# Kernel optimization log

Measured on AMD Instinct MI355X. Metric: run time of the kernel, lower is better.

Reference implementation:

```python
import jax, jax.numpy as jnp
import numpy as np

QLEN, MLEN, BSZ = 1024, 1024, 2
D_MODEL, N_HEAD, D_HEAD, D_INNER = 1024, 16, 64, 4096
KLEN = QLEN + MLEN
RLEN = KLEN + QLEN
EPS = 1e-12
SCALE = 1.0 / np.sqrt(D_HEAD).astype(np.float32)
STD = 0.02


def gelu(x):
    # OpenAI-GPT tanh-approx gelu used by XLNet
    return 0.5 * x * (1.0 + jnp.tanh(np.sqrt(2.0 / np.pi) * (x + 0.044715 * x ** 3)))


def layer_norm(x, g, b):
    m = jnp.mean(x, axis=-1, keepdims=True)
    v = jnp.mean((x - m) ** 2, axis=-1, keepdims=True)
    return (x - m) * jax.lax.rsqrt(v + EPS) * g + b


def rel_shift(x, klen):
    # x: [qlen, rlen, bsz, n_head] -> [qlen, klen, bsz, n_head]
    q, r, b, n = x.shape
    x = jnp.reshape(x, (r, q, b, n))[1:]
    x = jnp.reshape(x, (q, r - 1, b, n))[:, :klen]
    return x


def setup_inputs() -> dict:
    key = jax.random.key(0)
    ks = jax.random.split(key, 16)
    h = jax.random.normal(ks[0], (QLEN, BSZ, D_MODEL), jnp.float32)
    mems = jax.random.normal(ks[1], (MLEN, BSZ, D_MODEL), jnp.float32)
    r = jax.random.normal(ks[2], (RLEN, BSZ, D_MODEL), jnp.float32)
    # segment one-hot: 1 if query and key segments differ (XLNet convention)
    qseg = jax.random.randint(ks[3], (QLEN, BSZ), 0, 2)
    kseg = jax.random.randint(ks[4], (KLEN, BSZ), 0, 2)
    seg_mat = jax.nn.one_hot((qseg[:, None, :] != kseg[None, :, :]).astype(jnp.int32), 2, dtype=jnp.float32)  # [q,k,b,2]
    # causal mask with mems: query i may attend to key j <= i + MLEN
    i = jnp.arange(QLEN)[:, None]
    j = jnp.arange(KLEN)[None, :]
    attn_mask = (j > i + MLEN).astype(jnp.float32)[:, :, None, None]  # [q,k,1,1]
    wq = jax.random.normal(ks[5], (D_MODEL, N_HEAD, D_HEAD), jnp.float32) * STD
    wk = jax.random.normal(ks[6], (D_MODEL, N_HEAD, D_HEAD), jnp.float32) * STD
    wv = jax.random.normal(ks[7], (D_MODEL, N_HEAD, D_HEAD), jnp.float32) * STD
    wo = jax.random.normal(ks[8], (D_MODEL, N_HEAD, D_HEAD), jnp.float32) * STD
    wr = jax.random.normal(ks[9], (D_MODEL, N_HEAD, D_HEAD), jnp.float32) * STD
    r_w_bias = jnp.zeros((N_HEAD, D_HEAD), jnp.float32)
    r_r_bias = jnp.zeros((N_HEAD, D_HEAD), jnp.float32)
    r_s_bias = jnp.zeros((N_HEAD, D_HEAD), jnp.float32)
    seg_embed = jax.random.normal(ks[10], (2, N_HEAD, D_HEAD), jnp.float32) * STD
    ln_attn_g = jnp.ones((D_MODEL,), jnp.float32)
    ln_attn_b = jnp.zeros((D_MODEL,), jnp.float32)
    w1 = jax.random.normal(ks[11], (D_MODEL, D_INNER), jnp.float32) * STD
    b1 = jnp.zeros((D_INNER,), jnp.float32)
    w2 = jax.random.normal(ks[12], (D_INNER, D_MODEL), jnp.float32) * STD
    b2 = jnp.zeros((D_MODEL,), jnp.float32)
    ln_ff_g = jnp.ones((D_MODEL,), jnp.float32)
    ln_ff_b = jnp.zeros((D_MODEL,), jnp.float32)
    return dict(h=h, mems=mems, r=r, seg_mat=seg_mat, attn_mask=attn_mask,
                wq=wq, wk=wk, wv=wv, wo=wo, wr=wr,
                r_w_bias=r_w_bias, r_r_bias=r_r_bias, r_s_bias=r_s_bias, seg_embed=seg_embed,
                ln_attn_g=ln_attn_g, ln_attn_b=ln_attn_b,
                w1=w1, b1=b1, w2=w2, b2=b2, ln_ff_g=ln_ff_g, ln_ff_b=ln_ff_b)


def reference(h, mems, r, seg_mat, attn_mask, wq, wk, wv, wo, wr,
              r_w_bias, r_r_bias, r_s_bias, seg_embed,
              ln_attn_g, ln_attn_b, w1, b1, w2, b2, ln_ff_g, ln_ff_b):
    # content-stream XLNet relative attention (g=None path) + FFN
    cat = jnp.concatenate([mems, h], axis=0)            # [klen,b,h]
    q_h = jnp.einsum('ibh,hnd->ibnd', h, wq)
    k_h = jnp.einsum('ibh,hnd->ibnd', cat, wk)
    v_h = jnp.einsum('ibh,hnd->ibnd', cat, wv)
    k_r = jnp.einsum('ibh,hnd->ibnd', r, wr)
    ac = jnp.einsum('ibnd,jbnd->ijbn', q_h + r_w_bias, k_h)
    bd = jnp.einsum('ibnd,jbnd->ijbn', q_h + r_r_bias, k_r)
    bd = rel_shift(bd, KLEN)
    ef = jnp.einsum('ibnd,snd->ibns', q_h + r_s_bias, seg_embed)
    ef = jnp.einsum('ijbs,ibns->ijbn', seg_mat, ef)
    attn_score = (ac + bd + ef) * SCALE - 1e30 * attn_mask
    attn_prob = jax.nn.softmax(attn_score, axis=1)
    attn_vec = jnp.einsum('ijbn,jbnd->ibnd', attn_prob, v_h)
    attn_out = jnp.einsum('ibnd,hnd->ibh', attn_vec, wo) + h
    out_h = layer_norm(attn_out, ln_attn_g, ln_attn_b)
    ff = gelu(out_h @ w1 + b1) @ w2 + b2
    return layer_norm(ff + out_h, ln_ff_g, ln_ff_b)
```

## Files before the change

kernel.cpp:

```cpp
#include <hip/hip_runtime.h>
#include <hip/hip_bf16.h>


#define QLEN 1024
#define MLEN 1024
#define DM 1024
#define NH 16
#define DH 64
#define DI 4096
#define KLEN 2048
#define RLEN 3072

typedef __attribute__((ext_vector_type(8))) short s16x8;
typedef __attribute__((ext_vector_type(4))) float f32x4;
typedef unsigned short us;

__device__ __forceinline__ float bf2f(us u) {
    union { unsigned int i; float f; } x; x.i = ((unsigned int)u) << 16; return x.f;
}
__device__ __forceinline__ us f2bf(float f) {
    union { float f; unsigned int i; } x; x.f = f;
    return (us)((x.i + 0x7fffu + ((x.i >> 16) & 1u)) >> 16);
}
__device__ __forceinline__ void gload16(const void* g, void* lds) {
    __builtin_amdgcn_global_load_lds(
        (const __attribute__((address_space(1))) unsigned int*)g,
        (__attribute__((address_space(3))) unsigned int*)lds, 16, 0, 0);
}

template<bool ISMAX>
__device__ __forceinline__ float block_reduce(float v, float* red, int t) {
    #pragma unroll
    for (int off = 32; off > 0; off >>= 1) {
        float o = __shfl_down(v, off);
        v = ISMAX ? fmaxf(v, o) : (v + o);
    }
    if ((t & 63) == 0) red[t >> 6] = v;
    __syncthreads();
    if (t == 0) {
        float s = red[0];
        #pragma unroll
        for (int w = 1; w < 4; ++w) s = ISMAX ? fmaxf(s, red[w]) : (s + red[w]);
        red[4] = s;
    }
    __syncthreads();
    return red[4];
}

__global__ __launch_bounds__(256) void prep_k(
    const float* __restrict__ mems, const float* __restrict__ h,
    const float* __restrict__ r, const float* __restrict__ wo,
    const float* __restrict__ wq, const float* __restrict__ wk,
    const float* __restrict__ wv, const float* __restrict__ wr,
    const float* __restrict__ w1, const float* __restrict__ w2,
    const float* __restrict__ seg,
    us* __restrict__ cat_bf, us* __restrict__ r_bf, us* __restrict__ wo_b,
    us* __restrict__ wqkv_t, us* __restrict__ wr_t,
    us* __restrict__ w1_t, us* __restrict__ w2_t, us* __restrict__ ksb)
{
    __shared__ us tbuf[64][65];
    int bid = blockIdx.x;
    const int tid = threadIdx.x;
    if (bid < 5632) {
        int t = bid * 256 + tid;
        const float* src; us* dst; int off;
        if (t < 262144)       { src = mems; dst = cat_bf;           off = t; }
        else if (t < 524288)  { src = h;    dst = cat_bf + 2097152; off = t - 262144; }
        else if (t < 1310720) { src = r;    dst = r_bf;             off = t - 524288; }
        else                  { src = wo;   dst = wo_b;             off = t - 1310720; }
        const float4* p = (const float4*)src + 2 * (size_t)off;
        float4 a = p[0], b = p[1];
        us o[8] = { f2bf(a.x), f2bf(a.y), f2bf(a.z), f2bf(a.w),
                    f2bf(b.x), f2bf(b.y), f2bf(b.z), f2bf(b.w) };
        *((uint4*)dst + off) = *(const uint4*)o;
        return;
    }
    bid -= 5632;
    if (bid >= 3072) {
        int t = (bid - 3072) * 256 + tid;
        int bb = t >> 11, j = t & 2047;
        ksb[t] = f2bf(seg[(size_t)j * 4 + bb * 2 + 1]);
        return;
    }
    const float* in; us* out; int R, C, c0, r0;
    if (bid < 1024) {
        int z = bid >> 8, u = bid & 255;
        in  = (z == 0) ? wq : (z == 1) ? wk : (z == 2) ? wv : wr;
        out = (z < 3) ? (wqkv_t + (size_t)z * 1048576) : wr_t;
        R = 1024; C = 1024; c0 = (u & 15) * 64; r0 = (u >> 4) * 64;
    } else if (bid < 2048) {
        int u = bid - 1024;
        in = w1; out = w1_t; R = 1024; C = 4096;
        c0 = (u & 63) * 64; r0 = (u >> 6) * 64;
    } else {
        int u = bid - 2048;
        in = w2; out = w2_t; R = 4096; C = 1024;
        c0 = (u & 15) * 64; r0 = (u >> 4) * 64;
    }
    #pragma unroll
    for (int u = 0; u < 16; ++u) {
        int idx = tid + 256 * u;
        int rr = idx >> 6, cc = idx & 63;
        tbuf[cc][rr] = f2bf(in[(size_t)(r0 + rr) * C + c0 + cc]);
    }
    __syncthreads();
    #pragma unroll
    for (int u = 0; u < 16; ++u) {
        int idx = tid + 256 * u;
        int rr = idx >> 6, cc = idx & 63;
        out[(size_t)(c0 + rr) * R + r0 + cc] = tbuf[rr][cc];
    }
}

__device__ __forceinline__ int offe(int r, int c) {
    return ((r >> 4) * 2 + (c >> 5)) * 512 + (r & 15) * 32 + ((c & 31) ^ ((r & 8) ? 16 : 0));
}

template<int EPI>
__device__ __forceinline__ void gemm8_core(
    const us* __restrict__ A, const us* __restrict__ Bt,
    const float* __restrict__ bias, void* __restrict__ Cout,
    int N, int K, int kbeg, size_t zoff, bool zfirst,
    int bx, int by, us* __restrict__ As8, us* __restrict__ Bs8)
{
    const int tid = threadIdx.x;
    const int w = tid >> 6, l = tid & 63;
    const int lm = l & 15, lg = l >> 4;
    const int wm = w >> 2, wn = w & 3;
    const int m0 = by * 256, n0 = bx * 256;

    int srow[2], scol[2];
    #pragma unroll
    for (int u = 0; u < 2; ++u) {
        int sub = w * 2 + u;
        srow[u] = (sub >> 1) * 16 + (l >> 2);
        scol[u] = (sub & 1) * 32 + (((l & 3) * 8) ^ ((l & 32) ? 16 : 0));
    }

    auto stagePart = [&](int kt1, int P, int db) {
        const us* src = (P < 2) ? (A + (size_t)(m0 + P * 128) * K)
                                : (Bt + (size_t)(n0 + (P - 2) * 128) * K);
        us* dst = ((P < 2) ? As8 : Bs8) + (db * 2 + (P & 1)) * 8192;
        int kc = kbeg + kt1 * 64;
        #pragma unroll
        for (int u = 0; u < 2; ++u)
            gload16(src + (size_t)srow[u] * K + kc + scol[u], dst + (w * 2 + u) * 512);
    };

    f32x4 acc[8][4] = {};
    s16x8 rA0[4][2], rA1[4][2], rB[2][2];

    stagePart(0, 0, 0); stagePart(0, 1, 0); stagePart(0, 2, 0); stagePart(0, 3, 0);

    for (int kt = 0; kt < 16; ++kt) {
        const int d = kt & 1;
        asm volatile("s_waitcnt vmcnt(0)" ::: "memory");
        __builtin_amdgcn_s_barrier();
        asm volatile("" ::: "memory");
        const bool hn = (kt + 1 < 16);
        const us* Ab = As8 + (d * 2 + wm) * 8192;
        const us* Bb = Bs8 + (d * 2 + (wn >> 1)) * 8192;

        if (hn) stagePart(kt + 1, 0, d ^ 1);
        #pragma unroll
        for (int mf2 = 0; mf2 < 4; ++mf2)
            #pragma unroll
            for (int kk = 0; kk < 2; ++kk)
                rA0[mf2][kk] = *(const s16x8*)&Ab[offe(mf2 * 16 + lm, kk * 32 + lg * 8)];
        #pragma unroll
        for (int nf2 = 0; nf2 < 2; ++nf2)
            #pragma unroll
            for (int kk = 0; kk < 2; ++kk)
                rB[nf2][kk] = *(const s16x8*)&Bb[offe((wn & 1) * 64 + nf2 * 16 + lm, kk * 32 + lg * 8)];
        __builtin_amdgcn_s_setprio(1);
        #pragma unroll
        for (int mf2 = 0; mf2 < 4; ++mf2)
            #pragma unroll
            for (int nf2 = 0; nf2 < 2; ++nf2)
                #pragma unroll
                for (int kk = 0; kk < 2; ++kk)
                    acc[mf2][nf2] = __builtin_amdgcn_mfma_f32_16x16x32_bf16(
                        rA0[mf2][kk], rB[nf2][kk], acc[mf2][nf2], 0, 0, 0);
        __builtin_amdgcn_s_setprio(0);

        if (hn) stagePart(kt + 1, 1, d ^ 1);
        #pragma unroll
        for (int mf2 = 0; mf2 < 4; ++mf2)
            #pragma unroll
            for (int kk = 0; kk < 2; ++kk)
                rA1[mf2][kk] = *(const s16x8*)&Ab[offe(64 + mf2 * 16 + lm, kk * 32 + lg * 8)];
        __builtin_amdgcn_s_setprio(1);
        #pragma unroll
        for (int mf2 = 0; mf2 < 4; ++mf2)
            #pragma unroll
            for (int nf2 = 0; nf2 < 2; ++nf2)
                #pragma unroll
                for (int kk = 0; kk < 2; ++kk)
                    acc[4 + mf2][nf2] = __builtin_amdgcn_mfma_f32_16x16x32_bf16(
                        rA1[mf2][kk], rB[nf2][kk], acc[4 + mf2][nf2], 0, 0, 0);
        __builtin_amdgcn_s_setprio(0);

        if (hn) stagePart(kt + 1, 2, d ^ 1);
        #pragma unroll
        for (int nf2 = 0; nf2 < 2; ++nf2)
            #pragma unroll
            for (int kk = 0; kk < 2; ++kk)
                rB[nf2][kk] = *(const s16x8*)&Bb[offe((wn & 1) * 64 + (2 + nf2) * 16 + lm, kk * 32 + lg * 8)];
        __builtin_amdgcn_s_setprio(1);
        #pragma unroll
        for (int mf2 = 0; mf2 < 4; ++mf2)
            #pragma unroll
            for (int nf2 = 0; nf2 < 2; ++nf2)
                #pragma unroll
                for (int kk = 0; kk < 2; ++kk)
                    acc[4 + mf2][2 + nf2] = __builtin_amdgcn_mfma_f32_16x16x32_bf16(
                        rA1[mf2][kk], rB[nf2][kk], acc[4 + mf2][2 + nf2], 0, 0, 0);
        __builtin_amdgcn_s_setprio(0);

        if (hn) stagePart(kt + 1, 3, d ^ 1);
        __builtin_amdgcn_s_setprio(1);
        #pragma unroll
        for (int mf2 = 0; mf2 < 4; ++mf2)
            #pragma unroll
            for (int nf2 = 0; nf2 < 2; ++nf2)
                #pragma unroll
                for (int kk = 0; kk < 2; ++kk)
                    acc[mf2][2 + nf2] = __builtin_amdgcn_mfma_f32_16x16x32_bf16(
                        rA0[mf2][kk], rB[nf2][kk], acc[mf2][2 + nf2], 0, 0, 0);
        __builtin_amdgcn_s_setprio(0);
    }

    #pragma unroll
    for (int mf = 0; mf < 8; ++mf) {
        #pragma unroll
        for (int nf = 0; nf < 4; ++nf) {
            #pragma unroll
            for (int rr = 0; rr < 4; ++rr) {
                int row = m0 + wm * 128 + mf * 16 + lg * 4 + rr;
                int col = n0 + wn * 64 + nf * 16 + lm;
                float v = acc[mf][nf][rr];
                if (EPI == 3) {
                    int s = row >> 1, bb = row & 1, nn = col >> 6, dd = col & 63;
                    ((us*)Cout)[(((size_t)(bb * 16 + nn)) * RLEN + s) * 64 + dd] = f2bf(v);
                } else {
                    int which = col >> 10;
                    int nn = (col >> 6) & 15, dd = col & 63, bb = row & 1;
                    us val = f2bf(v);
                    us* base = (us*)Cout;
                    if (which == 0) {
                        if (row >= 2048)
                            base[(((size_t)(bb * 16 + nn)) * 1024 + ((row - 2048) >> 1)) * 64 + dd] = val;
                    } else if (which == 1) {
                        int j = row >> 1;
                        int jt = j >> 6, ff = (j >> 4) & 3, lmw = j & 15;
                        int ks2 = dd >> 5, lg2 = (dd >> 3) & 3, e2 = dd & 7;
                        (base + 2097152)[((((size_t)(bb * 16 + nn)) * 32 + jt) * 8 + ff * 2 + ks2) * 512
                                         + (lg2 * 16 + lmw) * 8 + e2] = val;
                    } else {
                        int j = row >> 1;
                        int jt = j >> 6, ks2 = (j >> 5) & 1, lg2 = (j >> 3) & 3, e2 = j & 7;
                        int df = dd >> 4, lmw = dd & 15;
                        (base + 6291456)[((((size_t)(bb * 16 + nn)) * 32 + jt) * 8 + df * 2 + ks2) * 512
                                         + (lg2 * 16 + lmw) * 8 + e2] = val;
                    }
                }
            }
        }
    }
}

__global__ __launch_bounds__(512) void proj8_k(
    const us* __restrict__ cat_bf, const us* __restrict__ wqkv_t,
    const us* __restrict__ r_bf, const us* __restrict__ wr_t,
    us* __restrict__ qkv_out, us* __restrict__ kr_out)
{
    __shared__ __align__(16) us As8[2 * 2 * 8192];
    __shared__ __align__(16) us Bs8[2 * 2 * 8192];
    int bid = blockIdx.x;
    if (bid < 192) {
        int swz = (bid & 7) * 24 + (bid >> 3);
        gemm8_core<4>(cat_bf, wqkv_t, nullptr, qkv_out, 3072, 1024, 0,
                      0, true, swz % 12, swz / 12, As8, Bs8);
    } else {
        int idx = bid - 192;
        gemm8_core<3>(r_bf, wr_t, nullptr, kr_out, 1024, 1024, 0,
                      0, true, idx % 4, idx / 4, As8, Bs8);
    }
}

template<int TM, int EPI>
__device__ __forceinline__ void gemm_core(
    const us* __restrict__ A, const us* __restrict__ Bt,
    const float* __restrict__ bias, void* __restrict__ Cout,
    int N, int K, int kbeg, int kchunk, size_t zoff, bool zfirst,
    int bx, int by, us* __restrict__ As, us* __restrict__ Bs)
{
    constexpr int MF = TM / 32;
    constexpr int AISS = TM / 64;
    const int tid = threadIdx.x;
    const int w = tid >> 6, l = tid & 63;
    const int lm = l & 15, lg = l >> 4;
    const int m0 = by * TM, n0 = bx * 128;
    const int wr = (w >> 1) * (TM / 2), wc = (w & 1) * 64;
    const int nt = kchunk / 32;

    f32x4 acc[MF][4] = {};

    auto stage = [&](int buf, int k0) {
        #pragma unroll
        for (int u = 0; u < AISS; ++u) {
            int c = (u * 4 + w) * 64 + l;
            int row = c & (TM - 1), kc = c >> (TM == 128 ? 7 : 6);
            gload16(A + (size_t)(m0 + row) * K + k0 + kc * 8,
                    As + buf * (TM * 32) + (u * 4 + w) * 512);
        }
        #pragma unroll
        for (int u = 0; u < 2; ++u) {
            int c = (u * 4 + w) * 64 + l;
            int row = c & 127, kc = c >> 7;
            gload16(Bt + (size_t)(n0 + row) * K + k0 + kc * 8,
                    Bs + buf * 4096 + (u * 4 + w) * 512);
        }
    };

    stage(0, kbeg);
    int cur = 0;
    for (int t = 0; t < nt; ++t) {
        asm volatile("s_waitcnt vmcnt(0)" ::: "memory");
        __builtin_amdgcn_s_barrier();
        asm volatile("" ::: "memory");
        if (t + 1 < nt) stage(cur ^ 1, kbeg + (t + 1) * 32);

        s16x8 af[MF], bfr[4];
        #pragma unroll
        for (int mf = 0; mf < MF; ++mf)
            af[mf] = *(const s16x8*)&As[cur * (TM * 32) + (lg * TM + wr + mf * 16 + lm) * 8];
        #pragma unroll
        for (int nf = 0; nf < 4; ++nf)
            bfr[nf] = *(const s16x8*)&Bs[cur * 4096 + (lg * 128 + wc + nf * 16 + lm) * 8];
        #pragma unroll
        for (int mf = 0; mf < MF; ++mf)
            #pragma unroll
            for (int nf = 0; nf < 4; ++nf)
                acc[mf][nf] = __builtin_amdgcn_mfma_f32_16x16x32_bf16(
                    af[mf], bfr[nf], acc[mf][nf], 0, 0, 0);
        cur ^= 1;
    }

    #pragma unroll
    for (int mf = 0; mf < MF; ++mf) {
        #pragma unroll
        for (int nf = 0; nf < 4; ++nf) {
            #pragma unroll
            for (int rr = 0; rr < 4; ++rr) {
                int row = m0 + wr + mf * 16 + lg * 4 + rr;
                int col = n0 + wc + nf * 16 + lm;
                float v = acc[mf][nf][rr];
                if (EPI == 1 || (EPI == 2 && zfirst)) v += bias[col];
                if (EPI == 1) {
                    float targ = 0.7978845608028654f * (v + 0.044715f * v * v * v);
                    v = 0.5f * v * (1.0f + tanhf(targ));
                    ((us*)Cout)[(size_t)row * N + col] = f2bf(v);
                } else {
                    ((float*)Cout + zoff)[(size_t)row * N + col] = v;
                }
            }
        }
    }
}

template<int TM, int EPI>
__global__ __launch_bounds__(256) void gemm2(
    const us* __restrict__ A, const us* __restrict__ Bt,
    const float* __restrict__ bias, void* __restrict__ Cout,
    int N, int K, int kchunk, size_t zstride)
{
    __shared__ us As[2 * TM * 32];
    __shared__ us Bs[2 * 128 * 32];
    int lin = blockIdx.y * gridDim.x + blockIdx.x;
    int nwg = gridDim.x * gridDim.y;
    int swz = (lin & 7) * (nwg >> 3) + (lin >> 3);
    int bx = swz % gridDim.x, by = swz / gridDim.x;
    gemm_core<TM, EPI>(A, Bt, bias, Cout, N, K, blockIdx.z * kchunk, kchunk,
                       (size_t)blockIdx.z * zstride, blockIdx.z == 0, bx, by, As, Bs);
}

__global__ __launch_bounds__(256) void attn8_k(
    const us* __restrict__ qb, const us* __restrict__ kfr, const us* __restrict__ vfr,
    const us* __restrict__ krb, const us* __restrict__ ksb,
    const float* __restrict__ rwb, const float* __restrict__ rrb,
    const float* __restrict__ rsb, const float* __restrict__ se,
    const float* __restrict__ seg,
    us* __restrict__ av)
{
    __shared__ us KR_lds[2][128 * 64];
    __shared__ float G_lds[4 * 80 * 20];
    __shared__ us P_lds[4 * 16 * 64];
    __shared__ us KS_lds[2048];
    __shared__ float Qx_lds[64][2];

    const int tid = threadIdx.x;
    const int w = tid >> 6, l = tid & 63;
    const int lm = l & 15, lg = l >> 4;
    int lin = blockIdx.y * gridDim.x + blockIdx.x;
    int swz = (lin & 7) * 64 + (lin >> 3);
    const int i0 = (swz & 15) * 64;
    const int bn = swz >> 4;
    const int b = bn >> 4, n = bn & 15;
    const int i = i0 + w * 16 + lm;

    const float SC = 0.125f * 1.44269504088896340736f;

    const us* kbase = kfr + (size_t)bn * 131072;
    const us* vbase = vfr + (size_t)bn * 131072;

    {
        const us* qrow = qb + ((size_t)bn * QLEN + i0 + l) * DH;
        s16x8 qv8[8];
        #pragma unroll
        for (int c = 0; c < 8; ++c) qv8[c] = *(const s16x8*)(qrow + c * 8);
        float e0 = 0.f, e1 = 0.f;
        #pragma unroll
        for (int c = 0; c < 8; ++c)
            #pragma unroll
            for (int e = 0; e < 8; ++e) {
                int d = c * 8 + e;
                float qv = bf2f((us)qv8[c][e]) + rsb[n * DH + d];
                e0 = fmaf(qv, se[(0 * NH + n) * DH + d], e0);
                e1 = fmaf(qv, se[(1 * NH + n) * DH + d], e1);
            }
        float qsI = seg[(size_t)(i0 + l) * 8192 + b * 2 + 1];
        float qs0 = seg[b * 2 + 1];
        float qs = (qsI != qs0) ? 1.f : 0.f;
        float ed = e1 - e0;
        if (w == 0) {
            Qx_lds[l][0] = (e0 + qs * ed) * SC;
            Qx_lds[l][1] = ed * (1.f - 2.f * qs) * SC;
        }
    }
    __syncthreads();

    s16x8 qwf[2], qrf[2], qxf;
    {
        const us* qrow = qb + ((size_t)bn * QLEN + i) * DH;
        #pragma unroll
        for (int ks = 0; ks < 2; ++ks) {
            s16x8 v = *(const s16x8*)(qrow + ks * 32 + lg * 8);
            #pragma unroll
            for (int e = 0; e < 8; ++e) {
                int d = ks * 32 + lg * 8 + e;
                float f = bf2f((us)v[e]);
                qwf[ks][e] = (short)f2bf((f + rwb[n * DH + d]) * SC);
                qrf[ks][e] = (short)f2bf((f + rrb[n * DH + d]) * SC);
            }
        }
        #pragma unroll
        for (int e = 0; e < 8; ++e) qxf[e] = 0;
        if (lg == 0) {
            qxf[0] = (short)f2bf(Qx_lds[w * 16 + lm][0]);
            qxf[1] = (short)f2bf(Qx_lds[w * 16 + lm][1]);
        }
    }

    auto stageKR = [&](int buf, int j0) {
        const int ur0 = QLEN - i0 - 63 + j0;
        #pragma unroll
        for (int u = 0; u < 4; ++u) {
            int c = (w * 4 + u) * 64 + l;
            int row = c >> 3, ch = c & 7;
            gload16(krb + ((size_t)bn * RLEN + ur0 + row) * DH + ((ch ^ (row & 7)) * 8),
                    &KR_lds[buf][(w * 4 + u) * 512]);
        }
    };

    int njt = ((i0 + 63 + MLEN) >> 6) + 1;
    if (njt > 32) njt = 32;

    gload16(ksb + b * KLEN + (w * 64 + l) * 8, &KS_lds[w * 512]);
    stageKR(0, 0);

    f32x4 of[4] = {{0,0,0,0},{0,0,0,0},{0,0,0,0},{0,0,0,0}};
    float M = -3.0e38f, L = 0.f;
    float* gw = &G_lds[w * 1600];
    us* pw = &P_lds[w * 1024];
    int cur = 0;

    for (int jt = 0; jt < njt; ++jt) {
        const int j0 = jt * 64;
        asm volatile("s_waitcnt vmcnt(0)" ::: "memory");
        __builtin_amdgcn_s_barrier();
        asm volatile("" ::: "memory");
        if (jt + 1 < njt) stageKR(cur ^ 1, j0 + 64);

        s16x8 kf[4][2], vf[4][2];
        #pragma unroll
        for (int f = 0; f < 4; ++f) {
            #pragma unroll
            for (int ks = 0; ks < 2; ++ks) {
                kf[f][ks] = *(const s16x8*)(kbase + (size_t)(((jt * 4 + f) * 2 + ks) * 64 + l) * 8);
                vf[f][ks] = *(const s16x8*)(vbase + (size_t)(((jt * 4 + f) * 2 + ks) * 64 + l) * 8);
            }
        }

        __builtin_amdgcn_s_setprio(1);
        const int woff = 48 - w * 16;
        #pragma unroll
        for (int pf = 0; pf < 5; ++pf) {
            f32x4 g = {0, 0, 0, 0};
            int row = woff + pf * 16 + lm;
            #pragma unroll
            for (int ks = 0; ks < 2; ++ks) {
                s16x8 a = *(const s16x8*)&KR_lds[cur][row * 64 + (((ks * 64 + lg * 16) ^ ((row & 7) << 4)) >> 1)];
                g = __builtin_amdgcn_mfma_f32_16x16x32_bf16(a, qrf[ks], g, 0, 0, 0);
            }
            #pragma unroll
            for (int rr = 0; rr < 4; ++rr)
                gw[(pf * 16 + lg * 4 + rr) * 20 + lm] = g[rr];
        }
        f32x4 sf[4];
        #pragma unroll
        for (int f = 0; f < 4; ++f) {
            f32x4 cfr = {0, 0, 0, 0};
            cfr = __builtin_amdgcn_mfma_f32_16x16x32_bf16(kf[f][0], qwf[0], cfr, 0, 0, 0);
            cfr = __builtin_amdgcn_mfma_f32_16x16x32_bf16(kf[f][1], qwf[1], cfr, 0, 0, 0);
            s16x8 aext;
            #pragma unroll
            for (int e = 0; e < 8; ++e) aext[e] = 0;
            if (lg == 0) {
                aext[0] = (short)0x3F80;
                aext[1] = (short)KS_lds[j0 + f * 16 + lm];
            }
            cfr = __builtin_amdgcn_mfma_f32_16x16x32_bf16(aext, qxf, cfr, 0, 0, 0);
            sf[f] = cfr;
        }
        __builtin_amdgcn_s_setprio(0);

        float sv[16];
        #pragma unroll
        for (int f = 0; f < 4; ++f)
            #pragma unroll
            for (int rr = 0; rr < 4; ++rr) {
                int jl = f * 16 + lg * 4 + rr;
                sv[f * 4 + rr] = sf[f][rr] + gw[(jl + 15 - lm) * 20 + lm];
            }
        if (j0 + 63 > i0 + w * 16 + MLEN) {
            #pragma unroll
            for (int f = 0; f < 4; ++f)
                #pragma unroll
                for (int rr = 0; rr < 4; ++rr) {
                    int jl = f * 16 + lg * 4 + rr;
                    if (j0 + jl > i + MLEN) sv[f * 4 + rr] = -1.0e30f;
                }
        }
        float tmax = sv[0];
        #pragma unroll
        for (int u = 1; u < 16; ++u) tmax = fmaxf(tmax, sv[u]);
        tmax = fmaxf(tmax, __shfl_xor(tmax, 16));
        tmax = fmaxf(tmax, __shfl_xor(tmax, 32));
        float Mnew = fmaxf(M, tmax);
        float scale;
        asm("v_exp_f32 %0, %1" : "=v"(scale) : "v"(M - Mnew));
        float psum = 0.f;
        unsigned int pk[8];
        #pragma unroll
        for (int f = 0; f < 4; ++f) {
            #pragma unroll
            for (int rp = 0; rp < 2; ++rp) {
                float p0, p1;
                asm("v_exp_f32 %0, %1" : "=v"(p0) : "v"(sv[f * 4 + rp * 2] - Mnew));
                asm("v_exp_f32 %0, %1" : "=v"(p1) : "v"(sv[f * 4 + rp * 2 + 1] - Mnew));
                psum += p0 + p1;
                unsigned int pkv;
                asm("v_cvt_pk_bf16_f32 %0, %1, %2" : "=v"(pkv) : "v"(p0), "v"(p1));
                pk[f * 2 + rp] = pkv;
            }
        }
        psum += __shfl_xor(psum, 16);
        psum += __shfl_xor(psum, 32);
        L = L * scale + psum;
        M = Mnew;
        float rs4[4];
        #pragma unroll
        for (int rr = 0; rr < 4; ++rr)
            rs4[rr] = __shfl(scale, (l & 48) | (lg * 4 + rr));
        #pragma unroll
        for (int df = 0; df < 4; ++df)
            #pragma unroll
            for (int rr = 0; rr < 4; ++rr)
                of[df][rr] *= rs4[rr];
        #pragma unroll
        for (int f = 0; f < 4; ++f) {
            #pragma unroll
            for (int rp = 0; rp < 2; ++rp) {
                int jl2 = f * 16 + lg * 4 + rp * 2;
                *(unsigned int*)&pw[lm * 64 + (((jl2 * 2) ^ ((lm & 7) << 4)) >> 1)] = pk[f * 2 + rp];
            }
        }
        __builtin_amdgcn_s_setprio(1);
        #pragma unroll
        for (int ks = 0; ks < 2; ++ks) {
            s16x8 pa = *(const s16x8*)&pw[lm * 64 + (((ks * 64 + lg * 16) ^ ((lm & 7) << 4)) >> 1)];
            #pragma unroll
            for (int df = 0; df < 4; ++df)
                of[df] = __builtin_amdgcn_mfma_f32_16x16x32_bf16(pa, vf[df][ks], of[df], 0, 0, 0);
        }
        __builtin_amdgcn_s_setprio(0);
        cur ^= 1;
    }

    float rl4[4];
    #pragma unroll
    for (int rr = 0; rr < 4; ++rr)
        rl4[rr] = __shfl(L, (l & 48) | (lg * 4 + rr));
    #pragma unroll
    for (int df = 0; df < 4; ++df) {
        #pragma unroll
        for (int rr = 0; rr < 4; ++rr) {
            int m2 = lg * 4 + rr;
            int d = df * 16 + lm;
            int irow = i0 + w * 16 + m2;
            av[((size_t)irow * 2 + b) * DM + n * DH + d] = f2bf(of[df][rr] / rl4[rr]);
        }
    }
}

template<int NSUM, bool RESBF, bool OUTBF>
__global__ __launch_bounds__(256) void ln_k(
    const float* __restrict__ a, const void* __restrict__ resid,
    const float* __restrict__ g, const float* __restrict__ bb,
    void* __restrict__ out)
{
    __shared__ float xs[DM];
    __shared__ float red[5];
    const int r = blockIdx.x;
    const int t = threadIdx.x;
    float lsum = 0.f;
    #pragma unroll
    for (int u = 0; u < 4; ++u) {
        int hdx = t + 256 * u;
        float x = RESBF ? bf2f(((const us*)resid)[(size_t)r * DM + hdx])
                        : ((const float*)resid)[(size_t)r * DM + hdx];
        #pragma unroll
        for (int s = 0; s < NSUM; ++s)
            x += a[(size_t)s * 2097152 + (size_t)r * DM + hdx];
        xs[hdx] = x;
        lsum += x;
    }
    float m = block_reduce<false>(lsum, red, t) * (1.0f / DM);
    float lv = 0.f;
    #pragma unroll
    for (int u = 0; u < 4; ++u) {
        int hdx = t + 256 * u;
        float dd = xs[hdx] - m;
        lv += dd * dd;
    }
    float var = block_reduce<false>(lv, red, t) * (1.0f / DM);
    float rs = rsqrtf(var + 1e-12f);
    #pragma unroll
    for (int u = 0; u < 4; ++u) {
        int hdx = t + 256 * u;
        float y = (xs[hdx] - m) * rs * g[hdx] + bb[hdx];
        if (OUTBF) ((us*)out)[(size_t)r * DM + hdx] = f2bf(y);
        else       ((float*)out)[(size_t)r * DM + hdx] = y;
    }
}

extern "C" void kernel_launch(void* const* d_in, const int* in_sizes, int n_in,
                              void* d_out, int out_size, void* d_ws, size_t ws_size,
                              hipStream_t stream) {
    const float* h         = (const float*)d_in[0];
    const float* mems      = (const float*)d_in[1];
    const float* r         = (const float*)d_in[2];
    const float* seg_mat   = (const float*)d_in[3];
    const float* wq        = (const float*)d_in[5];
    const float* wk        = (const float*)d_in[6];
    const float* wv        = (const float*)d_in[7];
    const float* wo        = (const float*)d_in[8];
    const float* wr        = (const float*)d_in[9];
    const float* rwb       = (const float*)d_in[10];
    const float* rrb       = (const float*)d_in[11];
    const float* rsb       = (const float*)d_in[12];
    const float* seg_embed = (const float*)d_in[13];
    const float* ln_g      = (const float*)d_in[14];
    const float* ln_b      = (const float*)d_in[15];
    const float* w1        = (const float*)d_in[16];
    const float* b1        = (const float*)d_in[17];
    const float* w2        = (const float*)d_in[18];
    const float* b2        = (const float*)d_in[19];
    const float* lf_g      = (const float*)d_in[20];
    const float* lf_b      = (const float*)d_in[21];
    float* out = (float*)d_out;
    char* W = (char*)d_ws;
    const size_t MB = 1ull << 20;

    us*    cat_bf = (us*)(W);
    us*    r_bf   = (us*)(W + 8  * MB);
    us*    wqkv_t = (us*)(W + 20 * MB);
    us*    wr_t   = (us*)(W + 26 * MB);
    us*    wo_b   = (us*)(W + 28 * MB);
    us*    w1_t   = (us*)(W + 30 * MB);
    us*    w2_t   = (us*)(W + 38 * MB);
    us*    q_bf   = (us*)(W + 46 * MB);
    us*    kfrag  = q_bf + 2097152;
    us*    vfrag  = q_bf + 6291456;
    us*    kr_bf  = (us*)(W + 66 * MB);
    us*    av_bf  = (us*)(W + 78 * MB);
    us*    ks_bf  = (us*)(W + 82 * MB);
    us*    oh_bf  = (us*)(W + 83 * MB);
    float* ao     = (float*)(W + 8 * MB);
    us*    ff1_bf = (us*)(W + 46 * MB);
    float* ff2    = (float*)(W);

    dim3 blk(256);
    dim3 blk8(512);
    prep_k<<<dim3(8720), blk, 0, stream>>>(mems, h, r, wo, wq, wk, wv, wr, w1, w2, seg_mat,
                                           cat_bf, r_bf, wo_b, wqkv_t, wr_t, w1_t, w2_t, ks_bf);
    proj8_k<<<dim3(260), blk8, 0, stream>>>(cat_bf, wqkv_t, r_bf, wr_t, q_bf, kr_bf);
    attn8_k<<<dim3(16, 32), blk, 0, stream>>>(q_bf, kfrag, vfrag, kr_bf, ks_bf,
                                              rwb, rrb, rsb, seg_embed, seg_mat, av_bf);
    gemm2<64, 0><<<dim3(8, 32, 2), blk, 0, stream>>>(av_bf, wo_b, nullptr, ao, 1024, 1024, 512, 2097152);
    ln_k<2, false, true><<<dim3(2048), blk, 0, stream>>>(ao, h, ln_g, ln_b, oh_bf);
    gemm2<128, 1><<<dim3(32, 16), blk, 0, stream>>>(oh_bf, w1_t, b1, ff1_bf, 4096, 1024, 1024, 0);
    gemm2<64, 2><<<dim3(8, 32, 4), blk, 0, stream>>>(ff1_bf, w2_t, b2, ff2, 1024, 4096, 1024, 2097152);
    ln_k<4, true, false><<<dim3(2048), blk, 0, stream>>>(ff2, oh_bf, lf_g, lf_b, out);
}
```

Before: 306.3 us.

## Write k_r in MFMA fragment layout and read it directly in attention

The r-projection epilogue now stores k_r pre-shuffled into 16-row MFMA fragment groups, offset by the rel-shift. The attention kernel can then load positional-key fragments straight from global memory, which removes the double-buffered LDS staging of k_r and its per-tile barriers. The attention grid is also flattened and reordered so paired blocks take complementary causal tile counts, for better load balance. The risk is that k_r fragments are now re-read from global/L2 by every block without LDS reuse, and the proj grid changes from 260 to 264 blocks.

```diff
diff --git a/kernel.cpp b/kernel.cpp
--- a/kernel.cpp
+++ b/kernel.cpp
@@ -241,7 +241,12 @@
                 float v = acc[mf][nf][rr];
                 if (EPI == 3) {
                     int s = row >> 1, bb = row & 1, nn = col >> 6, dd = col & 63;
-                    ((us*)Cout)[(((size_t)(bb * 16 + nn)) * RLEN + s) * 64 + dd] = f2bf(v);
+                    if (s >= 1) {
+                        int g = (s - 1) >> 4, lmw = (s - 1) & 15;
+                        int ks2 = dd >> 5, lg2 = (dd >> 3) & 3, e2 = dd & 7;
+                        ((us*)Cout)[((((size_t)(bb * 16 + nn)) * 144 + g) * 2 + ks2) * 512
+                                    + (lg2 * 16 + lmw) * 8 + e2] = f2bf(v);
+                    }
                 } else {
                     int which = col >> 10;
                     int nn = (col >> 6) & 15, dd = col & 63, bb = row & 1;
@@ -272,7 +277,7 @@
 __global__ __launch_bounds__(512) void proj8_k(
     const us* __restrict__ cat_bf, const us* __restrict__ wqkv_t,
     const us* __restrict__ r_bf, const us* __restrict__ wr_t,
-    us* __restrict__ qkv_out, us* __restrict__ kr_out)
+    us* __restrict__ qkv_out, us* __restrict__ krf_out)
 {
     __shared__ __align__(16) us As8[2 * 2 * 8192];
     __shared__ __align__(16) us Bs8[2 * 2 * 8192];
@@ -283,8 +288,8 @@
                       0, true, swz % 12, swz / 12, As8, Bs8);
     } else {
         int idx = bid - 192;
-        gemm8_core<3>(r_bf, wr_t, nullptr, kr_out, 1024, 1024, 0,
-                      0, true, idx % 4, idx / 4, As8, Bs8);
+        gemm8_core<3>(r_bf, wr_t, nullptr, krf_out, 1024, 1024, 0,
+                      0, true, idx & 3, idx >> 2, As8, Bs8);
     }
 }
 
@@ -385,15 +390,14 @@
                        (size_t)blockIdx.z * zstride, blockIdx.z == 0, bx, by, As, Bs);
 }
 
-__global__ __launch_bounds__(256) void attn8_k(
+__global__ __launch_bounds__(256) void attn9_k(
     const us* __restrict__ qb, const us* __restrict__ kfr, const us* __restrict__ vfr,
-    const us* __restrict__ krb, const us* __restrict__ ksb,
+    const us* __restrict__ krf, const us* __restrict__ ksb,
     const float* __restrict__ rwb, const float* __restrict__ rrb,
     const float* __restrict__ rsb, const float* __restrict__ se,
     const float* __restrict__ seg,
     us* __restrict__ av)
 {
-    __shared__ us KR_lds[2][128 * 64];
     __shared__ float G_lds[4 * 80 * 20];
     __shared__ us P_lds[4 * 16 * 64];
     __shared__ us KS_lds[2048];
@@ -402,10 +406,12 @@
     const int tid = threadIdx.x;
     const int w = tid >> 6, l = tid & 63;
     const int lm = l & 15, lg = l >> 4;
-    int lin = blockIdx.y * gridDim.x + blockIdx.x;
-    int swz = (lin & 7) * 64 + (lin >> 3);
-    const int i0 = (swz & 15) * 64;
-    const int bn = swz >> 4;
+    int lin = blockIdx.x;
+    int p = lin >> 1, parity = lin & 1;
+    const int bn = p >> 3;
+    int q = p & 7;
+    const int i0t = parity ? (15 - q) : q;
+    const int i0 = i0t * 64;
     const int b = bn >> 4, n = bn & 15;
     const int i = i0 + w * 16 + lm;
 
@@ -413,7 +419,9 @@
 
     const us* kbase = kfr + (size_t)bn * 131072;
     const us* vbase = vfr + (size_t)bn * 131072;
-
+    const us* krbase = krf + (size_t)bn * 147456;
+
+    gload16(ksb + b * KLEN + (w * 64 + l) * 8, &KS_lds[w * 512]);
     {
         const us* qrow = qb + ((size_t)bn * QLEN + i0 + l) * DH;
         s16x8 qv8[8];
@@ -438,6 +446,7 @@
             Qx_lds[l][1] = ed * (1.f - 2.f * qs) * SC;
         }
     }
+    asm volatile("s_waitcnt vmcnt(0)" ::: "memory");
     __syncthreads();
 
     s16x8 qwf[2], qrf[2], qxf;
@@ -462,35 +471,17 @@
         }
     }
 
-    auto stageKR = [&](int buf, int j0) {
-        const int ur0 = QLEN - i0 - 63 + j0;
-        #pragma unroll
-        for (int u = 0; u < 4; ++u) {
-            int c = (w * 4 + u) * 64 + l;
-            int row = c >> 3, ch = c & 7;
-            gload16(krb + ((size_t)bn * RLEN + ur0 + row) * DH + ((ch ^ (row & 7)) * 8),
-                    &KR_lds[buf][(w * 4 + u) * 512]);
-        }
-    };
-
     int njt = ((i0 + 63 + MLEN) >> 6) + 1;
     if (njt > 32) njt = 32;
-
-    gload16(ksb + b * KLEN + (w * 64 + l) * 8, &KS_lds[w * 512]);
-    stageKR(0, 0);
+    const int gq = 63 - (i0 >> 4) - w;
 
     f32x4 of[4] = {{0,0,0,0},{0,0,0,0},{0,0,0,0},{0,0,0,0}};
     float M = -3.0e38f, L = 0.f;
     float* gw = &G_lds[w * 1600];
     us* pw = &P_lds[w * 1024];
-    int cur = 0;
 
     for (int jt = 0; jt < njt; ++jt) {
         const int j0 = jt * 64;
-        asm volatile("s_waitcnt vmcnt(0)" ::: "memory");
-        __builtin_amdgcn_s_barrier();
-        asm volatile("" ::: "memory");
-        if (jt + 1 < njt) stageKR(cur ^ 1, j0 + 64);
 
         s16x8 kf[4][2], vf[4][2];
         #pragma unroll
@@ -503,19 +494,18 @@
         }
 
         __builtin_amdgcn_s_setprio(1);
-        const int woff = 48 - w * 16;
         #pragma unroll
         for (int pf = 0; pf < 5; ++pf) {
-            f32x4 g = {0, 0, 0, 0};
-            int row = woff + pf * 16 + lm;
+            int g = gq + 4 * jt + pf;
+            f32x4 gacc = {0, 0, 0, 0};
             #pragma unroll
             for (int ks = 0; ks < 2; ++ks) {
-                s16x8 a = *(const s16x8*)&KR_lds[cur][row * 64 + (((ks * 64 + lg * 16) ^ ((row & 7) << 4)) >> 1)];
-                g = __builtin_amdgcn_mfma_f32_16x16x32_bf16(a, qrf[ks], g, 0, 0, 0);
+                s16x8 a = *(const s16x8*)(krbase + (size_t)((g * 2 + ks) * 64 + l) * 8);
+                gacc = __builtin_amdgcn_mfma_f32_16x16x32_bf16(a, qrf[ks], gacc, 0, 0, 0);
             }
             #pragma unroll
             for (int rr = 0; rr < 4; ++rr)
-                gw[(pf * 16 + lg * 4 + rr) * 20 + lm] = g[rr];
+                gw[(pf * 16 + lg * 4 + rr) * 20 + lm] = gacc[rr];
         }
         f32x4 sf[4];
         #pragma unroll
@@ -605,7 +595,6 @@
                 of[df] = __builtin_amdgcn_mfma_f32_16x16x32_bf16(pa, vf[df][ks], of[df], 0, 0, 0);
         }
         __builtin_amdgcn_s_setprio(0);
-        cur ^= 1;
     }
 
     float rl4[4];
@@ -703,7 +692,7 @@
     us*    q_bf   = (us*)(W + 46 * MB);
     us*    kfrag  = q_bf + 2097152;
     us*    vfrag  = q_bf + 6291456;
-    us*    kr_bf  = (us*)(W + 66 * MB);
+    us*    krf    = (us*)(W + 66 * MB);
     us*    av_bf  = (us*)(W + 78 * MB);
     us*    ks_bf  = (us*)(W + 82 * MB);
     us*    oh_bf  = (us*)(W + 83 * MB);
@@ -715,9 +704,9 @@
     dim3 blk8(512);
     prep_k<<<dim3(8720), blk, 0, stream>>>(mems, h, r, wo, wq, wk, wv, wr, w1, w2, seg_mat,
                                            cat_bf, r_bf, wo_b, wqkv_t, wr_t, w1_t, w2_t, ks_bf);
-    proj8_k<<<dim3(260), blk8, 0, stream>>>(cat_bf, wqkv_t, r_bf, wr_t, q_bf, kr_bf);
-    attn8_k<<<dim3(16, 32), blk, 0, stream>>>(q_bf, kfrag, vfrag, kr_bf, ks_bf,
-                                              rwb, rrb, rsb, seg_embed, seg_mat, av_bf);
+    proj8_k<<<dim3(264), blk8, 0, stream>>>(cat_bf, wqkv_t, r_bf, wr_t, q_bf, krf);
+    attn9_k<<<dim3(512), blk, 0, stream>>>(q_bf, kfrag, vfrag, krf, ks_bf,
+                                           rwb, rrb, rsb, seg_embed, seg_mat, av_bf);
     gemm2<64, 0><<<dim3(8, 32, 2), blk, 0, stream>>>(av_bf, wo_b, nullptr, ao, 1024, 1024, 512, 2097152);
     ln_k<2, false, true><<<dim3(2048), blk, 0, stream>>>(ao, h, ln_g, ln_b, oh_bf);
     gemm2<128, 1><<<dim3(32, 16), blk, 0, stream>>>(oh_bf, w1_t, b1, ff1_bf, 4096, 1024, 1024, 0);
```

Measured after the change: 307.2 us. Within noise of the previous version (+0.3%).
